# Kernel optimization log

Hardware: AMD Instinct MI355X
Metric: run time of the kernel (lower is better)

## Reference

```python
import jax, jax.numpy as jnp
import numpy as np
from jax import lax

WS = 7          # window size
SHIFT = WS // 2 # shift for odd blocks
NH = 4          # num heads
PATCH = 4


def _rel_index(ws):
    # standard Swin relative position index, shape (ws*ws, ws*ws)
    coords = np.stack(np.meshgrid(np.arange(ws), np.arange(ws), indexing='ij')).reshape(2, -1)
    rel = (coords[:, :, None] - coords[:, None, :]).transpose(1, 2, 0)
    rel[..., 0] += ws - 1
    rel[..., 1] += ws - 1
    rel[..., 0] *= 2 * ws - 1
    return jnp.asarray(rel.sum(-1))


def _attn_mask(H, W, ws, s):
    # BasicLayer mask for cyclic shift: (nW, ws*ws, ws*ws) with 0 / -100
    img = np.zeros((H, W))
    cnt = 0
    for hs in (slice(0, -ws), slice(-ws, -s), slice(-s, None)):
        for wsl in (slice(0, -ws), slice(-ws, -s), slice(-s, None)):
            img[hs, wsl] = cnt
            cnt += 1
    mw = img.reshape(H // ws, ws, W // ws, ws).transpose(0, 2, 1, 3).reshape(-1, ws * ws)
    diff = mw[:, None, :] - mw[:, :, None]
    return jnp.asarray(np.where(diff != 0, -100.0, 0.0).astype(np.float32))


def setup_inputs() -> dict:
    key = jax.random.key(0)
    ks = jax.random.split(key, 6)
    C = 128
    return {
        'x': jax.random.normal(ks[0], (16, 3, 448, 448), jnp.float32),
        'conv_w': jax.random.normal(ks[1], (C, 3, PATCH, PATCH), jnp.float32) * 0.02,
        'conv_b': jnp.zeros((C,), jnp.float32),
        'qkv_w': jax.random.normal(ks[2], (2, 3 * C, C), jnp.float32) * 0.02,
        'qkv_b': jnp.zeros((2, 3 * C), jnp.float32),
        'proj_w': jax.random.normal(ks[3], (2, C, C), jnp.float32) * 0.02,
        'proj_b': jnp.zeros((2, C), jnp.float32),
        'rpb': jax.random.normal(ks[4], (2, (2 * WS - 1) ** 2, NH), jnp.float32) * 0.02,
    }


def _forward(x, conv_w, conv_b, qkv_w, qkv_b, proj_w, proj_b, rpb):
    # patch embed: strided conv
    y = lax.conv_general_dilated(x, conv_w, (PATCH, PATCH), 'VALID',
                                 dimension_numbers=('NCHW', 'OIHW', 'NCHW'))
    y = y + conv_b[None, :, None, None]
    B, C, H, W = y.shape
    hd = C // NH
    scale = hd ** -0.5
    N = WS * WS
    nW = (H // WS) * (W // WS)
    t = y.reshape(B, C, H * W).transpose(0, 2, 1)  # (B, L, C)

    rel_idx = _rel_index(WS)                    # (N, N)
    mask = _attn_mask(H, W, WS, SHIFT)          # (nW, N, N)

    for i in range(2):
        shift = 0 if i % 2 == 0 else SHIFT
        xw = t.reshape(B, H, W, C)
        if shift > 0:
            xw = jnp.roll(xw, (-shift, -shift), axis=(1, 2))
        # window partition -> (B*nW, N, C)
        win = xw.reshape(B, H // WS, WS, W // WS, WS, C).transpose(0, 1, 3, 2, 4, 5).reshape(-1, N, C)
        qkv = win @ qkv_w[i].T + qkv_b[i]       # (B*nW, N, 3C)
        qkv = qkv.reshape(-1, N, 3, NH, hd).transpose(2, 0, 3, 1, 4)
        q, k, v = qkv[0], qkv[1], qkv[2]        # (B*nW, NH, N, hd)
        attn = jnp.einsum('wnid,wnjd->wnij', q * scale, k)
        bias = rpb[i][rel_idx].transpose(2, 0, 1)  # (NH, N, N)
        attn = attn + bias[None]
        if shift > 0:
            attn = (attn.reshape(B, nW, NH, N, N) + mask[None, :, None]).reshape(-1, NH, N, N)
        attn = jax.nn.softmax(attn, axis=-1)
        out = jnp.einsum('wnij,wnjd->wnid', attn, v).transpose(0, 2, 1, 3).reshape(-1, N, C)
        out = out @ proj_w[i].T + proj_b[i]
        # window reverse
        xw = out.reshape(B, H // WS, W // WS, WS, WS, C).transpose(0, 1, 3, 2, 4, 5).reshape(B, H, W, C)
        if shift > 0:
            xw = jnp.roll(xw, (shift, shift), axis=(1, 2))
        t = xw.reshape(B, H * W, C)

    return t.reshape(B, H, W, C).transpose(0, 3, 1, 2)  # (B, C, H, W)


def reference(x, conv_w, conv_b, qkv_w, qkv_b, proj_w, proj_b, rpb):
    return _forward(x, conv_w, conv_b, qkv_w, qkv_b, proj_w, proj_b, rpb)
```

## Files before the change

kernel.cpp:

```cpp
#include <hip/hip_runtime.h>

#define BB 16
#define CC 128
#define HH 112
#define NHH 4
#define WSZ 7
#define NN 49
#define SH 3

typedef _Float16 h8 __attribute__((ext_vector_type(8)));
typedef _Float16 h4 __attribute__((ext_vector_type(4)));
typedef float f4 __attribute__((ext_vector_type(4)));

__device__ __forceinline__ int rid3(int p) { return p < 105 ? 0 : (p < 109 ? 1 : 2); }

#define SWZ(row, j, CH) ((row) * ((CH) * 8) + (((((j) >> 3) ^ (row)) & ((CH) - 1)) << 3) + ((j) & 7))

__device__ __forceinline__ h4 pack4(f4 v) {
  h4 r; r[0] = (_Float16)v[0]; r[1] = (_Float16)v[1];
  r[2] = (_Float16)v[2]; r[3] = (_Float16)v[3];
  return r;
}

__device__ __forceinline__ h8 xpose(h4 p0, h4 p1, int lg, int li) {
  int sl0 = li + ((lg & 1) << 5);
  int sl1 = sl0 + 16;
  int2 a = *(int2*)&p0, b = *(int2*)&p1;
  int d0a = __shfl(a.x, sl0, 64), d0b = __shfl(b.x, sl0, 64);
  int d1a = __shfl(a.y, sl0, 64), d1b = __shfl(b.y, sl0, 64);
  int d2a = __shfl(a.x, sl1, 64), d2b = __shfl(b.x, sl1, 64);
  int d3a = __shfl(a.y, sl1, 64), d3b = __shfl(b.y, sl1, 64);
  bool hi = (lg & 2) != 0;
  int4 r = make_int4(hi ? d0b : d0a, hi ? d1b : d1a, hi ? d2b : d2a, hi ? d3b : d3a);
  return *(h8*)&r;
}

__global__ __launch_bounds__(256) void conv_embed(const float* __restrict__ x,
    const float* __restrict__ cw, const float* __restrict__ cb, _Float16* __restrict__ t0) {
  __shared__ float xs[3][4][448];
  __shared__ float wT[48][128];
  __shared__ float cbs[128];
  int bid = blockIdx.x;
  int b = bid / HH, oh = bid % HH;
  int tid = threadIdx.x;
  for (int idx = tid; idx < 3 * 4 * 448; idx += 256) {
    int ch = idx / 1792;
    int r = (idx / 448) & 3;
    int col = idx % 448;
    xs[ch][r][col] = x[((b * 3 + ch) * 448 + (oh * 4 + r)) * 448 + col];
  }
  for (int idx = tid; idx < 6144; idx += 256) {
    int c = idx / 48, k = idx - c * 48;
    wT[k][c] = cw[idx];
  }
  if (tid < 128) cbs[tid] = cb[tid];
  __syncthreads();
  int c0 = (tid & 31) << 2;
  int gg = tid >> 5;
  for (int it = 0; it < 4; ++it) {
    int gw0 = it * 32 + gg * 4;
    if (gw0 >= HH) break;
    float acc[4][4] = {};
#pragma unroll
    for (int k = 0; k < 48; ++k) {
      int ch = k >> 4, r = (k >> 2) & 3, j = k & 3;
      float4 wv = *(const float4*)&wT[k][c0];
#pragma unroll
      for (int d = 0; d < 4; ++d) {
        float xv = xs[ch][r][(gw0 + d) * 4 + j];
        acc[d][0] = fmaf(xv, wv.x, acc[d][0]);
        acc[d][1] = fmaf(xv, wv.y, acc[d][1]);
        acc[d][2] = fmaf(xv, wv.z, acc[d][2]);
        acc[d][3] = fmaf(xv, wv.w, acc[d][3]);
      }
    }
    float4 bv = *(const float4*)&cbs[c0];
#pragma unroll
    for (int d = 0; d < 4; ++d) {
      int gw = gw0 + d;
      h4 o;
      o[0] = (_Float16)(acc[d][0] + bv.x); o[1] = (_Float16)(acc[d][1] + bv.y);
      o[2] = (_Float16)(acc[d][2] + bv.z); o[3] = (_Float16)(acc[d][3] + bv.w);
      *(h4*)&t0[((size_t)(b * HH + oh) * HH + gw) * CC + c0] = o;
    }
  }
}

__global__ void prep(const float* __restrict__ qw, const float* __restrict__ qb,
                     const float* __restrict__ pw, const float* __restrict__ rpb,
                     _Float16* __restrict__ qwh, float* __restrict__ qbs,
                     _Float16* __restrict__ pwh, float* __restrict__ biasT) {
  const float scale = 0.17677669529663687f;
  int tid0 = blockIdx.x * blockDim.x + threadIdx.x;
  int stride = gridDim.x * blockDim.x;
  for (int idx = tid0; idx < 2 * 384 * 128; idx += stride) {
    int n = (idx >> 7) % 384;
    float v = qw[idx];
    if (n < 128) v *= scale;
    qwh[idx] = (_Float16)v;
  }
  for (int idx = tid0; idx < 2 * 384; idx += stride) {
    int n = idx % 384;
    float v = qb[idx];
    if (n < 128) v *= scale;
    qbs[idx] = v;
  }
  for (int idx = tid0; idx < 2 * 128 * 128; idx += stride)
    pwh[idx] = (_Float16)pw[idx];
  for (int idx = tid0; idx < 2 * 4 * 4 * 4 * 64 * 4; idx += stride) {
    int r = idx & 3;
    int lane = (idx >> 2) & 63;
    int it = (idx >> 8) & 3;
    int jt = (idx >> 10) & 3;
    int hh = (idx >> 12) & 3;
    int ll = idx >> 14;
    int i = it * 16 + (lane & 15);
    int j = jt * 16 + ((lane >> 4) * 4) + r;
    float v = 0.f;
    if (i < NN && j < NN) {
      int rel = ((i / 7 - j / 7) + 6) * 13 + ((i % 7 - j % 7) + 6);
      v = rpb[(ll * 169 + rel) * NHH + hh];
    }
    biasT[idx] = v;
  }
}

__global__ __launch_bounds__(256, 4) void swin_layer(
    const _Float16* __restrict__ tin, _Float16* __restrict__ toutB, float* __restrict__ outN,
    const _Float16* __restrict__ qwh, const float* __restrict__ qbs,
    const _Float16* __restrict__ pwh, const float* __restrict__ pb,
    const float* __restrict__ biasT, int shift, int writeN) {
  __shared__ _Float16 sm[16384];

  int tid = threadIdx.x;
  int wid = blockIdx.x;
  int b = wid >> 8;
  int wh = (wid >> 4) & 15, ww = wid & 15;
  int w = tid >> 6, l = tid & 63, li = l & 15, lg = l >> 4;
  int h = w;

  for (int c = tid; c < 64 * 16; c += 256) {
    int n = c >> 4, k0 = (c & 15) * 8;
    int gh = wh * WSZ + n / 7 + shift; if (gh >= HH) gh -= HH;
    int gw = ww * WSZ + n % 7 + shift; if (gw >= HH) gw -= HH;
    h8 v = *(const h8*)(tin + ((size_t)(b * HH + gh) * HH + gw) * CC + k0);
    *(h8*)&sm[SWZ(n, k0, 16)] = v;
  }
  __syncthreads();

  {
    f4 acc[2][4];
#pragma unroll
    for (int half = 0; half < 2; ++half) {
      float4 bb = *(const float4*)&qbs[256 + h * 32 + half * 16 + lg * 4];
#pragma unroll
      for (int nt = 0; nt < 4; ++nt) acc[half][nt] = f4{bb.x, bb.y, bb.z, bb.w};
    }
#pragma unroll
    for (int ks = 0; ks < 4; ++ks) {
      h8 bW[4];
#pragma unroll
      for (int nt = 0; nt < 4; ++nt)
        bW[nt] = *(const h8*)&sm[SWZ(nt * 16 + li, ks * 32 + lg * 8, 16)];
#pragma unroll
      for (int half = 0; half < 2; ++half) {
        int mt = 16 + 2 * h + half;
        h8 a = *(const h8*)(qwh + (size_t)(mt * 16 + li) * 128 + ks * 32 + lg * 8);
#pragma unroll
        for (int nt = 0; nt < 4; ++nt)
          acc[half][nt] = __builtin_amdgcn_mfma_f32_16x16x32_f16(a, bW[nt], acc[half][nt], 0, 0, 0);
      }
    }
#pragma unroll
    for (int half = 0; half < 2; ++half)
#pragma unroll
      for (int nt = 0; nt < 4; ++nt) {
        int i = nt * 16 + li;
#pragma unroll
        for (int r = 0; r < 4; ++r)
          sm[8192 + h * 2048 + SWZ(half * 16 + lg * 4 + r, i, 8)] = (_Float16)acc[half][nt][r];
      }
  }

  h8 Kf[4], Qf[4];
  {
    f4 accK[2][4], accQ[2][4];
#pragma unroll
    for (int half = 0; half < 2; ++half) {
      float4 bk = *(const float4*)&qbs[128 + h * 32 + half * 16 + lg * 4];
      float4 bq = *(const float4*)&qbs[h * 32 + half * 16 + lg * 4];
#pragma unroll
      for (int nt = 0; nt < 4; ++nt) {
        accK[half][nt] = f4{bk.x, bk.y, bk.z, bk.w};
        accQ[half][nt] = f4{bq.x, bq.y, bq.z, bq.w};
      }
    }
#pragma unroll
    for (int ks = 0; ks < 4; ++ks) {
      h8 bW[4];
#pragma unroll
      for (int nt = 0; nt < 4; ++nt)
        bW[nt] = *(const h8*)&sm[SWZ(nt * 16 + li, ks * 32 + lg * 8, 16)];
#pragma unroll
      for (int half = 0; half < 2; ++half) {
        h8 aK = *(const h8*)(qwh + (size_t)((8 + 2 * h + half) * 16 + li) * 128 + ks * 32 + lg * 8);
        h8 aQ = *(const h8*)(qwh + (size_t)((2 * h + half) * 16 + li) * 128 + ks * 32 + lg * 8);
#pragma unroll
        for (int nt = 0; nt < 4; ++nt) {
          accK[half][nt] = __builtin_amdgcn_mfma_f32_16x16x32_f16(aK, bW[nt], accK[half][nt], 0, 0, 0);
          accQ[half][nt] = __builtin_amdgcn_mfma_f32_16x16x32_f16(aQ, bW[nt], accQ[half][nt], 0, 0, 0);
        }
      }
    }
#pragma unroll
    for (int t = 0; t < 4; ++t) {
      Kf[t] = xpose(pack4(accK[0][t]), pack4(accK[1][t]), lg, li);
      Qf[t] = xpose(pack4(accQ[0][t]), pack4(accQ[1][t]), lg, li);
    }
  }

  float inv[4];
  h4 P4[4][4];
  {
    f4 s[4][4];
    const float* bT = biasT + h * 4096;
#pragma unroll
    for (int jt = 0; jt < 4; ++jt)
#pragma unroll
      for (int it = 0; it < 4; ++it)
        s[jt][it] = *(const f4*)&bT[(jt * 4 + it) * 256 + l * 4];
    __builtin_amdgcn_s_setprio(1);
#pragma unroll
    for (int jt = 0; jt < 4; ++jt)
#pragma unroll
      for (int it = 0; it < 4; ++it)
        s[jt][it] = __builtin_amdgcn_mfma_f32_16x16x32_f16(Kf[jt], Qf[it], s[jt][it], 0, 0, 0);
    __builtin_amdgcn_s_setprio(0);
#pragma unroll
    for (int jt = 0; jt < 4; ++jt)
#pragma unroll
      for (int it = 0; it < 4; ++it)
#pragma unroll
        for (int r = 0; r < 4; ++r) {
          int j = jt * 16 + lg * 4 + r;
          s[jt][it][r] = (j < NN) ? s[jt][it][r] : -1e30f;
        }
    if (shift && (wh == 15 || ww == 15)) {
      int regi[4], regj[4][4];
#pragma unroll
      for (int it = 0; it < 4; ++it) {
        int i = it * 16 + li;
        regi[it] = rid3(wh * WSZ + i / 7) * 3 + rid3(ww * WSZ + i % 7);
      }
#pragma unroll
      for (int jt = 0; jt < 4; ++jt)
#pragma unroll
        for (int r = 0; r < 4; ++r) {
          int j = jt * 16 + lg * 4 + r;
          regj[jt][r] = rid3(wh * WSZ + j / 7) * 3 + rid3(ww * WSZ + j % 7);
        }
#pragma unroll
      for (int jt = 0; jt < 4; ++jt)
#pragma unroll
        for (int it = 0; it < 4; ++it)
#pragma unroll
          for (int r = 0; r < 4; ++r)
            if (regj[jt][r] != regi[it]) s[jt][it][r] -= 100.f;
    }
#pragma unroll
    for (int it = 0; it < 4; ++it) {
      float mx = -1e30f;
#pragma unroll
      for (int jt = 0; jt < 4; ++jt)
#pragma unroll
        for (int r = 0; r < 4; ++r) mx = fmaxf(mx, s[jt][it][r]);
      mx = fmaxf(mx, __shfl_xor(mx, 16));
      mx = fmaxf(mx, __shfl_xor(mx, 32));
      float sum = 0.f;
#pragma unroll
      for (int jt = 0; jt < 4; ++jt)
#pragma unroll
        for (int r = 0; r < 4; ++r) {
          float e = __expf(s[jt][it][r] - mx);
          s[jt][it][r] = e;
          sum += e;
        }
      sum += __shfl_xor(sum, 16);
      sum += __shfl_xor(sum, 32);
      inv[it] = 1.f / sum;
    }
#pragma unroll
    for (int jt = 0; jt < 4; ++jt)
#pragma unroll
      for (int it = 0; it < 4; ++it)
        P4[jt][it] = pack4(s[jt][it]);
  }

  {
    h8 aV[2][2];
#pragma unroll
    for (int mt = 0; mt < 2; ++mt)
#pragma unroll
      for (int ks = 0; ks < 2; ++ks)
        aV[mt][ks] = *(const h8*)&sm[8192 + h * 2048 + SWZ(mt * 16 + li, ks * 32 + lg * 8, 8)];
    h8 bP[4][2];
#pragma unroll
    for (int nt = 0; nt < 4; ++nt)
#pragma unroll
      for (int ks = 0; ks < 2; ++ks)
        bP[nt][ks] = xpose(P4[2 * ks][nt], P4[2 * ks + 1][nt], lg, li);
    f4 o[2][4] = {};
    __builtin_amdgcn_s_setprio(1);
#pragma unroll
    for (int ks = 0; ks < 2; ++ks)
#pragma unroll
      for (int mt = 0; mt < 2; ++mt)
#pragma unroll
        for (int nt = 0; nt < 4; ++nt)
          o[mt][nt] = __builtin_amdgcn_mfma_f32_16x16x32_f16(aV[mt][ks], bP[nt][ks], o[mt][nt], 0, 0, 0);
    __builtin_amdgcn_s_setprio(0);
    __syncthreads();
#pragma unroll
    for (int mt = 0; mt < 2; ++mt)
#pragma unroll
      for (int nt = 0; nt < 4; ++nt) {
        int i = nt * 16 + li;
        int d = h * 32 + mt * 16 + lg * 4;
        float is = inv[nt];
        h4 v = {(_Float16)(o[mt][nt][0] * is), (_Float16)(o[mt][nt][1] * is),
                (_Float16)(o[mt][nt][2] * is), (_Float16)(o[mt][nt][3] * is)};
        *(h4*)&sm[SWZ(i, d, 16)] = v;
      }
  }
  __syncthreads();

  {
    f4 acc[2][4];
#pragma unroll
    for (int mi = 0; mi < 2; ++mi) {
      float4 bb = *(const float4*)&pb[(w * 2 + mi) * 16 + lg * 4];
#pragma unroll
      for (int nt = 0; nt < 4; ++nt) acc[mi][nt] = f4{bb.x, bb.y, bb.z, bb.w};
    }
#pragma unroll
    for (int ks = 0; ks < 4; ++ks) {
      h8 bO[4];
#pragma unroll
      for (int nt = 0; nt < 4; ++nt)
        bO[nt] = *(const h8*)&sm[SWZ(nt * 16 + li, ks * 32 + lg * 8, 16)];
#pragma unroll
      for (int mi = 0; mi < 2; ++mi) {
        int mt = w * 2 + mi;
        h8 a = *(const h8*)(pwh + (size_t)(mt * 16 + li) * 128 + ks * 32 + lg * 8);
#pragma unroll
        for (int nt = 0; nt < 4; ++nt)
          acc[mi][nt] = __builtin_amdgcn_mfma_f32_16x16x32_f16(a, bO[nt], acc[mi][nt], 0, 0, 0);
      }
    }
    if (!writeN) {
#pragma unroll
      for (int mi = 0; mi < 2; ++mi) {
        int dbase = (w * 2 + mi) * 16 + lg * 4;
#pragma unroll
        for (int nt = 0; nt < 4; ++nt) {
          int i = nt * 16 + li;
          h4 v = {(_Float16)acc[mi][nt][0], (_Float16)acc[mi][nt][1],
                  (_Float16)acc[mi][nt][2], (_Float16)acc[mi][nt][3]};
          *(h4*)&sm[8192 + SWZ(i, dbase, 16)] = v;
        }
      }
      __syncthreads();
      for (int cidx = tid; cidx < NN * 16; cidx += 256) {
        int tok = cidx >> 4, c = cidx & 15;
        h8 v = *(const h8*)&sm[8192 + SWZ(tok, c * 8, 16)];
        int gh = wh * WSZ + tok / 7;
        int gw = ww * WSZ + tok % 7;
        *(h8*)&toutB[((size_t)(b * HH + gh) * HH + gw) * CC + c * 8] = v;
      }
    } else {
#pragma unroll
      for (int mi = 0; mi < 2; ++mi) {
        int dbase = (w * 2 + mi) * 16 + lg * 4;
#pragma unroll
        for (int nt = 0; nt < 4; ++nt) {
          int i = nt * 16 + li;
          if (i < NN) {
            int gh = wh * WSZ + i / 7 + shift; if (gh >= HH) gh -= HH;
            int gw = ww * WSZ + i % 7 + shift; if (gw >= HH) gw -= HH;
            size_t bse = ((size_t)(b * CC + dbase) * HH + gh) * HH + gw;
            outN[bse] = acc[mi][nt][0];
            outN[bse + (size_t)HH * HH] = acc[mi][nt][1];
            outN[bse + (size_t)2 * HH * HH] = acc[mi][nt][2];
            outN[bse + (size_t)3 * HH * HH] = acc[mi][nt][3];
          }
        }
      }
    }
  }
}

extern "C" void kernel_launch(void* const* d_in, const int* in_sizes, int n_in,
                              void* d_out, int out_size, void* d_ws, size_t ws_size,
                              hipStream_t stream) {
  const float* x = (const float*)d_in[0];
  const float* cw = (const float*)d_in[1];
  const float* cb = (const float*)d_in[2];
  const float* qkvw = (const float*)d_in[3];
  const float* qkvb = (const float*)d_in[4];
  const float* projw = (const float*)d_in[5];
  const float* projb = (const float*)d_in[6];
  const float* rpb = (const float*)d_in[7];
  float* out = (float*)d_out;

  char* ws = (char*)d_ws;
  _Float16* t0 = (_Float16*)ws;
  size_t off = (size_t)BB * HH * HH * CC * 2;
  _Float16* qwh = (_Float16*)(ws + off);  off += 2 * 384 * 128 * 2;
  _Float16* pwh = (_Float16*)(ws + off);  off += 2 * 128 * 128 * 2;
  float* qbs = (float*)(ws + off);        off += 2 * 384 * 4;
  float* biasT = (float*)(ws + off);

  prep<<<224, 256, 0, stream>>>(qkvw, qkvb, projw, rpb, qwh, qbs, pwh, biasT);
  conv_embed<<<BB * HH, 256, 0, stream>>>(x, cw, cb, t0);

  swin_layer<<<4096, 256, 0, stream>>>(t0, t0, nullptr,
      qwh, qbs, pwh, projb, biasT, 0, 0);
  swin_layer<<<4096, 256, 0, stream>>>(t0, nullptr, out,
      qwh + 384 * 128, qbs + 384, pwh + 128 * 128, projb + 128,
      biasT + 16384, SH, 1);
}
```

Measured before the change: 288.0 us.

## Split K/Q projection to cut register pressure, store bias in fp16, raise occupancy

The fused K and Q projection loops are split into two sequential blocks, so only one set of eight accumulators is live at a time, which lowers VGPR pressure. The relative-position bias table is now stored and loaded as fp16 instead of fp32, halving that read traffic. Launch bounds rise from 4 to 5 blocks per SM to exploit the lower register use. The trade-offs are less MFMA interleaving between the K and Q chains, a small loss of bias precision, and possible spills under the tighter register cap.

```diff
diff --git a/kernel.cpp b/kernel.cpp
--- a/kernel.cpp
+++ b/kernel.cpp
@@ -89,7 +89,7 @@
 __global__ void prep(const float* __restrict__ qw, const float* __restrict__ qb,
                      const float* __restrict__ pw, const float* __restrict__ rpb,
                      _Float16* __restrict__ qwh, float* __restrict__ qbs,
-                     _Float16* __restrict__ pwh, float* __restrict__ biasT) {
+                     _Float16* __restrict__ pwh, _Float16* __restrict__ biasT) {
   const float scale = 0.17677669529663687f;
   int tid0 = blockIdx.x * blockDim.x + threadIdx.x;
   int stride = gridDim.x * blockDim.x;
@@ -121,15 +121,15 @@
       int rel = ((i / 7 - j / 7) + 6) * 13 + ((i % 7 - j % 7) + 6);
       v = rpb[(ll * 169 + rel) * NHH + hh];
     }
-    biasT[idx] = v;
-  }
-}
-
-__global__ __launch_bounds__(256, 4) void swin_layer(
+    biasT[idx] = (_Float16)v;
+  }
+}
+
+__global__ __launch_bounds__(256, 5) void swin_layer(
     const _Float16* __restrict__ tin, _Float16* __restrict__ toutB, float* __restrict__ outN,
     const _Float16* __restrict__ qwh, const float* __restrict__ qbs,
     const _Float16* __restrict__ pwh, const float* __restrict__ pb,
-    const float* __restrict__ biasT, int shift, int writeN) {
+    const _Float16* __restrict__ biasT, int shift, int writeN) {
   __shared__ _Float16 sm[16384];
 
   int tid = threadIdx.x;
@@ -184,16 +184,12 @@
 
   h8 Kf[4], Qf[4];
   {
-    f4 accK[2][4], accQ[2][4];
+    f4 acc[2][4];
 #pragma unroll
     for (int half = 0; half < 2; ++half) {
       float4 bk = *(const float4*)&qbs[128 + h * 32 + half * 16 + lg * 4];
-      float4 bq = *(const float4*)&qbs[h * 32 + half * 16 + lg * 4];
-#pragma unroll
-      for (int nt = 0; nt < 4; ++nt) {
-        accK[half][nt] = f4{bk.x, bk.y, bk.z, bk.w};
-        accQ[half][nt] = f4{bq.x, bq.y, bq.z, bq.w};
-      }
+#pragma unroll
+      for (int nt = 0; nt < 4; ++nt) acc[half][nt] = f4{bk.x, bk.y, bk.z, bk.w};
     }
 #pragma unroll
     for (int ks = 0; ks < 4; ++ks) {
@@ -203,32 +199,55 @@
         bW[nt] = *(const h8*)&sm[SWZ(nt * 16 + li, ks * 32 + lg * 8, 16)];
 #pragma unroll
       for (int half = 0; half < 2; ++half) {
-        h8 aK = *(const h8*)(qwh + (size_t)((8 + 2 * h + half) * 16 + li) * 128 + ks * 32 + lg * 8);
-        h8 aQ = *(const h8*)(qwh + (size_t)((2 * h + half) * 16 + li) * 128 + ks * 32 + lg * 8);
-#pragma unroll
-        for (int nt = 0; nt < 4; ++nt) {
-          accK[half][nt] = __builtin_amdgcn_mfma_f32_16x16x32_f16(aK, bW[nt], accK[half][nt], 0, 0, 0);
-          accQ[half][nt] = __builtin_amdgcn_mfma_f32_16x16x32_f16(aQ, bW[nt], accQ[half][nt], 0, 0, 0);
-        }
-      }
-    }
-#pragma unroll
-    for (int t = 0; t < 4; ++t) {
-      Kf[t] = xpose(pack4(accK[0][t]), pack4(accK[1][t]), lg, li);
-      Qf[t] = xpose(pack4(accQ[0][t]), pack4(accQ[1][t]), lg, li);
-    }
+        h8 a = *(const h8*)(qwh + (size_t)((8 + 2 * h + half) * 16 + li) * 128 + ks * 32 + lg * 8);
+#pragma unroll
+        for (int nt = 0; nt < 4; ++nt)
+          acc[half][nt] = __builtin_amdgcn_mfma_f32_16x16x32_f16(a, bW[nt], acc[half][nt], 0, 0, 0);
+      }
+    }
+#pragma unroll
+    for (int t = 0; t < 4; ++t)
+      Kf[t] = xpose(pack4(acc[0][t]), pack4(acc[1][t]), lg, li);
+  }
+  {
+    f4 acc[2][4];
+#pragma unroll
+    for (int half = 0; half < 2; ++half) {
+      float4 bq = *(const float4*)&qbs[h * 32 + half * 16 + lg * 4];
+#pragma unroll
+      for (int nt = 0; nt < 4; ++nt) acc[half][nt] = f4{bq.x, bq.y, bq.z, bq.w};
+    }
+#pragma unroll
+    for (int ks = 0; ks < 4; ++ks) {
+      h8 bW[4];
+#pragma unroll
+      for (int nt = 0; nt < 4; ++nt)
+        bW[nt] = *(const h8*)&sm[SWZ(nt * 16 + li, ks * 32 + lg * 8, 16)];
+#pragma unroll
+      for (int half = 0; half < 2; ++half) {
+        h8 a = *(const h8*)(qwh + (size_t)((2 * h + half) * 16 + li) * 128 + ks * 32 + lg * 8);
+#pragma unroll
+        for (int nt = 0; nt < 4; ++nt)
+          acc[half][nt] = __builtin_amdgcn_mfma_f32_16x16x32_f16(a, bW[nt], acc[half][nt], 0, 0, 0);
+      }
+    }
+#pragma unroll
+    for (int t = 0; t < 4; ++t)
+      Qf[t] = xpose(pack4(acc[0][t]), pack4(acc[1][t]), lg, li);
   }
 
   float inv[4];
   h4 P4[4][4];
   {
     f4 s[4][4];
-    const float* bT = biasT + h * 4096;
+    const _Float16* bT = biasT + h * 4096;
 #pragma unroll
     for (int jt = 0; jt < 4; ++jt)
 #pragma unroll
-      for (int it = 0; it < 4; ++it)
-        s[jt][it] = *(const f4*)&bT[(jt * 4 + it) * 256 + l * 4];
+      for (int it = 0; it < 4; ++it) {
+        h4 bb = *(const h4*)&bT[(jt * 4 + it) * 256 + l * 4];
+        s[jt][it] = f4{(float)bb[0], (float)bb[1], (float)bb[2], (float)bb[3]};
+      }
     __builtin_amdgcn_s_setprio(1);
 #pragma unroll
     for (int jt = 0; jt < 4; ++jt)
@@ -418,7 +437,7 @@
   _Float16* qwh = (_Float16*)(ws + off);  off += 2 * 384 * 128 * 2;
   _Float16* pwh = (_Float16*)(ws + off);  off += 2 * 128 * 128 * 2;
   float* qbs = (float*)(ws + off);        off += 2 * 384 * 4;
-  float* biasT = (float*)(ws + off);
+  _Float16* biasT = (_Float16*)(ws + off);
 
   prep<<<224, 256, 0, stream>>>(qkvw, qkvb, projw, rpb, qwh, qbs, pwh, biasT);
   conv_embed<<<BB * HH, 256, 0, stream>>>(x, cw, cb, t0);
```

Measured after the change: 407.4 us. 1.41x slower.
